# Kernel tuning notes

Hardware: AMD Instinct MI355X
Metric: run time of the kernel (lower is better)

Reference implementation:

```python
import jax, jax.numpy as jnp
import numpy as np
import math

B, N, DIM = 4, 2048, 512
HEADS, DIM_HEAD = 8, 64
INNER = HEADS * DIM_HEAD  # 512


def setup_inputs() -> dict:
    key = jax.random.key(0)
    ks = jax.random.split(key, 4)
    x = jax.random.normal(ks[0], (B, N, DIM), dtype=jnp.float32)
    # nn.Linear(dim, inner*4, bias=False): store as [dim, 4*inner] for x @ W
    w_qkvg = jax.random.normal(ks[1], (DIM, 4 * INNER), dtype=jnp.float32) * (1.0 / math.sqrt(DIM))
    sigma = jnp.full((1, HEADS, 1, 1), 1.92, dtype=jnp.float32)
    w_out = jax.random.normal(ks[2], (2 * INNER, DIM), dtype=jnp.float32) * (1.0 / math.sqrt(2 * INNER))
    b_out = jax.random.normal(ks[3], (DIM,), dtype=jnp.float32) * 0.01
    return {"x": x, "w_qkvg": w_qkvg, "sigma": sigma, "w_out": w_out, "b_out": b_out}


def reference(x, w_qkvg, sigma, w_out, b_out):
    b, n, d = x.shape
    h, dh = HEADS, DIM_HEAD
    scale = dh ** (-0.5)

    qkvg = x @ w_qkvg  # [b, n, 4*inner]
    q, k, vg, vsigma = jnp.split(qkvg, 4, axis=-1)

    def to_heads(t):  # [b, n, h*dh] -> [b, h, n, dh]
        return t.reshape(b, n, h, dh).transpose(0, 2, 1, 3)

    q, k, vg, vsigma = map(to_heads, (q, k, vg, vsigma))

    # --- softmax branch ---
    dots = jnp.einsum('bhid,bhjd->bhij', q, k) * scale  # [b, h, n, n]
    corr_g = jax.nn.softmax(dots, axis=-1)
    out_g = jnp.matmul(corr_g, vg)  # [b, h, n, dh]

    # --- Gaussian positional-mask branch ---
    pos = jnp.arange(1, n + 1, dtype=x.dtype)
    diffs = jnp.abs(pos[:, None] - pos[None, :])  # [n, n]
    inv_norm = 1.0 / (jnp.sqrt(jnp.asarray(2.0 * math.pi, x.dtype)) * sigma)  # [1, h, 1, 1]
    gm = inv_norm * jnp.exp(-(diffs ** 2)[None, None] / (2.0 * sigma ** 2))  # [1, h, n, n]
    corr_sigma = gm / gm.sum(-1, keepdims=True)
    out_s = jnp.matmul(corr_sigma, vsigma)  # broadcasts over batch -> [b, h, n, dh]

    out = jnp.concatenate([out_g, out_s], axis=-1)  # [b, h, n, 2*dh]
    out = out.transpose(0, 2, 1, 3).reshape(b, n, 2 * h * dh)
    return out @ w_out + b_out
```

## Files before the change

### kernel.cpp

```cpp
#include <hip/hip_runtime.h>

typedef _Float16 f16;
typedef __attribute__((ext_vector_type(8))) _Float16 f16x8;
typedef __attribute__((ext_vector_type(4))) _Float16 f16x4;
typedef __attribute__((ext_vector_type(4))) float f32x4;

#define B_ 4
#define N_ 2048
#define DIM_ 512
#define H_ 8
#define DH_ 64

__device__ __forceinline__ void gload16(const void* g, void* l) {
    __builtin_amdgcn_global_load_lds((const __attribute__((address_space(1))) void*)g,
                                     (__attribute__((address_space(3))) void*)l, 16, 0, 0);
}


__global__ __launch_bounds__(256) void cvt_f16_k8(const float* __restrict__ in,
                                                  f16* __restrict__ out, int n8) {
    int i = blockIdx.x * 256 + threadIdx.x;
    if (i < n8) {
        const float4 a = ((const float4*)in)[i * 2];
        const float4 b = ((const float4*)in)[i * 2 + 1];
        f16x8 o = {(f16)a.x, (f16)a.y, (f16)a.z, (f16)a.w,
                   (f16)b.x, (f16)b.y, (f16)b.z, (f16)b.w};
        ((f16x8*)out)[i] = o;
    }
}

__global__ __launch_bounds__(256) void transpose_cvt_k(const float* __restrict__ in,
                                                       f16* __restrict__ out, int K, int N) {
    __shared__ f16 tile[64][72];
    const int nbk = K >> 6;
    const int bk = blockIdx.x % nbk, bn = blockIdx.x / nbk;
    const int k0 = bk << 6, n0 = bn << 6;
    const int t = threadIdx.x;
    const int r = t >> 2, q = (t & 3) << 4;
#pragma unroll
    for (int u = 0; u < 4; u++) {
        const float4 v = *(const float4*)&in[(size_t)(k0 + r) * N + n0 + q + u * 4];
        tile[q + u * 4 + 0][r] = (f16)v.x;
        tile[q + u * 4 + 1][r] = (f16)v.y;
        tile[q + u * 4 + 2][r] = (f16)v.z;
        tile[q + u * 4 + 3][r] = (f16)v.w;
    }
    __syncthreads();
#pragma unroll
    for (int u = 0; u < 2; u++) {
        f16x8 o = *(const f16x8*)&tile[r][q + u * 8];
        *(f16x8*)&out[(size_t)(n0 + r) * K + k0 + q + u * 8] = o;
    }
}

__global__ __launch_bounds__(256) void gemm_bt0(
    const f16* __restrict__ A, const f16* __restrict__ BT, int K, int N,
    f16* __restrict__ qb, f16* __restrict__ kb, f16* __restrict__ vbT,
    f16* __restrict__ vs16)
{
    __shared__ char sAb[16384];
    __shared__ char sBb[16384];
    const int tid = threadIdx.x;
    const int bid = blockIdx.x;
    const int xcd = bid & 7, w = bid >> 3;
    const int m0 = ((xcd << 3) + (w >> 4)) << 7;
    const int n0 = (w & 15) << 7;
    const int wave = tid >> 6, lane = tid & 63;
    const int wr = wave >> 1, wc = wave & 1;
    const int lr = lane & 15, lg = lane >> 4;

    f32x4 acc[4][4];
    const f32x4 zero = {0.f, 0.f, 0.f, 0.f};
#pragma unroll
    for (int i = 0; i < 4; i++)
#pragma unroll
        for (int j = 0; j < 4; j++) acc[i][j] = zero;

    const f16* srcA[4]; const f16* srcB[4];
    char* ldsA[4]; char* ldsB[4];
#pragma unroll
    for (int u = 0; u < 4; u++) {
        int row = wave * 8 + u * 32 + (lane >> 3);
        int e0 = ((lane & 7) ^ (row & 7)) << 3;
        srcA[u] = A + (size_t)(m0 + row) * K + e0;
        srcB[u] = BT + (size_t)(n0 + row) * K + e0;
        ldsA[u] = sAb + wave * 1024 + u * 4096;
        ldsB[u] = sBb + wave * 1024 + u * 4096;
    }

    const int swz = (lr & 7) << 4;
    for (int kt = 0; kt < K; kt += 64) {
#pragma unroll
        for (int u = 0; u < 4; u++) {
            gload16(srcA[u], ldsA[u]);
            gload16(srcB[u], ldsB[u]);
            srcA[u] += 64; srcB[u] += 64;
        }
        __syncthreads();
#pragma unroll
        for (int half = 0; half < 2; half++) {
            f16x8 af[4], bf[4];
#pragma unroll
            for (int i = 0; i < 4; i++) {
                int R = wr * 64 + i * 16 + lr;
                af[i] = *(const f16x8*)(sAb + R * 128 + (((half << 6) | (lg << 4)) ^ swz));
            }
#pragma unroll
            for (int j = 0; j < 4; j++) {
                int R = wc * 64 + j * 16 + lr;
                bf[j] = *(const f16x8*)(sBb + R * 128 + (((half << 6) | (lg << 4)) ^ swz));
            }
#pragma unroll
            for (int i = 0; i < 4; i++)
#pragma unroll
                for (int j = 0; j < 4; j++)
                    acc[i][j] = __builtin_amdgcn_mfma_f32_16x16x32_f16(af[i], bf[j], acc[i][j], 0, 0, 0);
        }
        __syncthreads();
    }

#pragma unroll
    for (int i = 0; i < 4; i++) {
#pragma unroll
        for (int j = 0; j < 4; j++) {
            int col = n0 + wc * 64 + j * 16 + lr;
            int row0 = m0 + wr * 64 + i * 16 + lg * 4;
            int sec = col >> 9, cc = col & 511;
            int h = cc >> 6, d = cc & 63;
            int b = row0 >> 11, ns = row0 & 2047;
            if (sec == 2) {
                f16x4 o;
#pragma unroll
                for (int r = 0; r < 4; r++) o[r] = (f16)acc[i][j][r];
                *(f16x4*)&vbT[((size_t)(b * H_ + h) * DH_ + d) * N_ + ns] = o;
            } else if (sec == 0) {
#pragma unroll
                for (int r = 0; r < 4; r++)
                    qb[((size_t)(b * H_ + h) * N_ + ns + r) * DH_ + d] = (f16)(acc[i][j][r] * 0.1803368801f);
            } else if (sec == 1) {
#pragma unroll
                for (int r = 0; r < 4; r++)
                    kb[((size_t)(b * H_ + h) * N_ + ns + r) * DH_ + d] = (f16)acc[i][j][r];
            } else {
#pragma unroll
                for (int r = 0; r < 4; r++)
                    vs16[((size_t)(b * H_ + h) * N_ + ns + r) * DH_ + d] = (f16)acc[i][j][r];
            }
        }
    }
}

__global__ __launch_bounds__(256) void gemm_small(
    const f16* __restrict__ A, const f16* __restrict__ BT, int K, int N,
    const float* __restrict__ bias, float* __restrict__ outp)
{
    __shared__ char sAb[8192];
    __shared__ char sBb[8192];
    const int tid = threadIdx.x;
    const int bid = blockIdx.x;
    const int xcd = bid & 7, w = bid >> 3;
    const int m0 = ((xcd << 4) + (w >> 3)) << 6;
    const int n0 = (w & 7) << 6;
    const int wave = tid >> 6, lane = tid & 63;
    const int wr = wave >> 1, wc = wave & 1;
    const int lr = lane & 15, lg = lane >> 4;

    f32x4 acc[2][2];
    const f32x4 zero = {0.f, 0.f, 0.f, 0.f};
#pragma unroll
    for (int i = 0; i < 2; i++)
#pragma unroll
        for (int j = 0; j < 2; j++) acc[i][j] = zero;

    const f16* srcA[2]; const f16* srcB[2];
    char* ldsA[2]; char* ldsB[2];
#pragma unroll
    for (int u = 0; u < 2; u++) {
        int row = wave * 8 + u * 32 + (lane >> 3);
        int e0 = ((lane & 7) ^ (row & 7)) << 3;
        srcA[u] = A + (size_t)(m0 + row) * K + e0;
        srcB[u] = BT + (size_t)(n0 + row) * K + e0;
        ldsA[u] = sAb + wave * 1024 + u * 4096;
        ldsB[u] = sBb + wave * 1024 + u * 4096;
    }

    const int swz = (lr & 7) << 4;
    for (int kt = 0; kt < K; kt += 64) {
#pragma unroll
        for (int u = 0; u < 2; u++) {
            gload16(srcA[u], ldsA[u]);
            gload16(srcB[u], ldsB[u]);
            srcA[u] += 64; srcB[u] += 64;
        }
        __syncthreads();
#pragma unroll
        for (int half = 0; half < 2; half++) {
            f16x8 af[2], bf[2];
#pragma unroll
            for (int i = 0; i < 2; i++) {
                int R = wr * 32 + i * 16 + lr;
                af[i] = *(const f16x8*)(sAb + R * 128 + (((half << 6) | (lg << 4)) ^ swz));
            }
#pragma unroll
            for (int j = 0; j < 2; j++) {
                int R = wc * 32 + j * 16 + lr;
                bf[j] = *(const f16x8*)(sBb + R * 128 + (((half << 6) | (lg << 4)) ^ swz));
            }
#pragma unroll
            for (int i = 0; i < 2; i++)
#pragma unroll
                for (int j = 0; j < 2; j++)
                    acc[i][j] = __builtin_amdgcn_mfma_f32_16x16x32_f16(af[i], bf[j], acc[i][j], 0, 0, 0);
        }
        __syncthreads();
    }

#pragma unroll
    for (int i = 0; i < 2; i++)
#pragma unroll
        for (int j = 0; j < 2; j++) {
            int col = n0 + wc * 32 + j * 16 + lr;
            int row0 = m0 + wr * 32 + i * 16 + lg * 4;
#pragma unroll
            for (int r = 0; r < 4; r++)
                outp[(size_t)(row0 + r) * N + col] = acc[i][j][r] + bias[col];
        }
}

__global__ __launch_bounds__(256) void attn_k(
    const f16* __restrict__ qb, const f16* __restrict__ kb, const f16* __restrict__ vbT,
    f16* __restrict__ cat, f16* __restrict__ oaccB, float* __restrict__ lacc)
{
    __shared__ char sKbf[2 * 8192];
    __shared__ char sVbf[2 * 8192];
    const int tid = threadIdx.x;
    const int bid0 = blockIdx.x;
    const int obid = (bid0 & 7) * 128 + (bid0 >> 3);
    const int bh = obid >> 5, qblk = (obid >> 1) & 15, half = obid & 1;
    const int b = bh >> 3, h = bh & 7;
    const int hn = half << 4;
    const int wave = tid >> 6, lane = tid & 63;
    const int lr = lane & 15, lg = lane >> 4;

    const size_t base = (size_t)bh * N_ * DH_;
    const int qrow_a = qblk * 128 + wave * 32 + lr;
    const int qrow_b = qrow_a + 16;
    const f16x8 qfa0 = *(const f16x8*)&qb[base + (size_t)qrow_a * DH_ + lg * 8];
    const f16x8 qfa1 = *(const f16x8*)&qb[base + (size_t)qrow_a * DH_ + 32 + lg * 8];
    const f16x8 qfb0 = *(const f16x8*)&qb[base + (size_t)qrow_b * DH_ + lg * 8];
    const f16x8 qfb1 = *(const f16x8*)&qb[base + (size_t)qrow_b * DH_ + 32 + lg * 8];

    const f16* kq[2]; const f16* vq[2];
#pragma unroll
    for (int u = 0; u < 2; u++) {
        int row = wave * 8 + u * 32 + (lane >> 3);
        int e0 = ((lane & 7) ^ (row & 7)) << 3;
        kq[u] = kb + base + (size_t)row * 64 + e0;
        vq[u] = vbT + base + (size_t)row * 2048 + e0;
    }
    char* const ldsKw = sKbf + wave * 1024;
    char* const ldsVw = sVbf + wave * 1024;

    f32x4 Ota[4], Otb[4], lacc_a, lacc_b;
    const f32x4 zero = {0.f, 0.f, 0.f, 0.f};
#pragma unroll
    for (int dt = 0; dt < 4; dt++) { Ota[dt] = zero; Otb[dt] = zero; }
    lacc_a = zero; lacc_b = zero;
    const f16x8 ones8 = {(f16)1.f, (f16)1.f, (f16)1.f, (f16)1.f,
                         (f16)1.f, (f16)1.f, (f16)1.f, (f16)1.f};

    const int swz = (lr & 7) << 4;

#pragma unroll
    for (int u = 0; u < 2; u++) gload16(kq[u] + (size_t)hn * 4096, ldsKw + u * 4096);
#pragma unroll
    for (int u = 0; u < 2; u++) gload16(vq[u] + hn * 64, ldsVw + u * 4096);
    asm volatile("s_waitcnt vmcnt(0)" ::: "memory");
    __builtin_amdgcn_s_barrier();

    for (int t = 0; t < 16; t++) {
        {
            const int tn = hn + ((t + 1) & 15);
            char* vdst = ldsVw + ((t + 1) & 1) * 8192;
            char* kdst = ldsKw + ((t + 1) & 1) * 8192;
#pragma unroll
            for (int u = 0; u < 2; u++) gload16(vq[u] + tn * 64, vdst + u * 4096);
#pragma unroll
            for (int u = 0; u < 2; u++) gload16(kq[u] + (size_t)tn * 4096, kdst + u * 4096);
        }

        const char* Kb = sKbf + (t & 1) * 8192;
        const char* Vb = sVbf + (t & 1) * 8192;

        f32x4 sta[4], stb[4];
        __builtin_amdgcn_s_setprio(1);
#pragma unroll
        for (int ct = 0; ct < 4; ct++) {
            int row = ct * 16 + lr;
            f16x8 kf0 = *(const f16x8*)(Kb + (((row << 7) | (lg << 4)) ^ swz));
            f16x8 kf1 = *(const f16x8*)(Kb + (((row << 7) | 64 | (lg << 4)) ^ swz));
            f32x4 sa = __builtin_amdgcn_mfma_f32_16x16x32_f16(kf0, qfa0, zero, 0, 0, 0);
            sta[ct]  = __builtin_amdgcn_mfma_f32_16x16x32_f16(kf1, qfa1, sa, 0, 0, 0);
            f32x4 sb = __builtin_amdgcn_mfma_f32_16x16x32_f16(kf0, qfb0, zero, 0, 0, 0);
            stb[ct]  = __builtin_amdgcn_mfma_f32_16x16x32_f16(kf1, qfb1, sb, 0, 0, 0);
        }
        __builtin_amdgcn_s_setprio(0);

        f16x4 ppa[4], ppb[4];
#pragma unroll
        for (int ct = 0; ct < 4; ct++)
#pragma unroll
            for (int r = 0; r < 4; r++) {
                ppa[ct][r] = (f16)__builtin_amdgcn_exp2f(sta[ct][r]);
                ppb[ct][r] = (f16)__builtin_amdgcn_exp2f(stb[ct][r]);
            }

        __builtin_amdgcn_s_setprio(1);
#pragma unroll
        for (int c = 0; c < 2; c++) {
            f16x8 bfa = __builtin_shufflevector(ppa[2 * c], ppa[2 * c + 1], 0, 1, 2, 3, 4, 5, 6, 7);
            f16x8 bfb = __builtin_shufflevector(ppb[2 * c], ppb[2 * c + 1], 0, 1, 2, 3, 4, 5, 6, 7);
            lacc_a = __builtin_amdgcn_mfma_f32_16x16x32_f16(ones8, bfa, lacc_a, 0, 0, 0);
            lacc_b = __builtin_amdgcn_mfma_f32_16x16x32_f16(ones8, bfb, lacc_b, 0, 0, 0);
#pragma unroll
            for (int dt = 0; dt < 4; dt++) {
                int row = dt * 16 + lr;
                f16x4 vlo = *(const f16x4*)(Vb + (((row << 7) | (c << 6) | (lg << 3)) ^ swz));
                f16x4 vhi = *(const f16x4*)(Vb + (((row << 7) | (c << 6) | 32 | (lg << 3)) ^ swz));
                f16x8 vf = __builtin_shufflevector(vlo, vhi, 0, 1, 2, 3, 4, 5, 6, 7);
                Ota[dt] = __builtin_amdgcn_mfma_f32_16x16x32_f16(vf, bfa, Ota[dt], 0, 0, 0);
                Otb[dt] = __builtin_amdgcn_mfma_f32_16x16x32_f16(vf, bfb, Otb[dt], 0, 0, 0);
            }
        }
        __builtin_amdgcn_s_setprio(0);

        asm volatile("s_waitcnt vmcnt(0)" ::: "memory");
        __builtin_amdgcn_s_barrier();
    }

#pragma unroll
    for (int dt = 0; dt < 4; dt++) {
        f16x4 oa, ob;
#pragma unroll
        for (int r = 0; r < 4; r++) {
            oa[r] = (f16)Ota[dt][r];
            ob[r] = (f16)Otb[dt][r];
        }
        if (half == 0) {
            *(f16x4*)&cat[((size_t)(b * N_ + qrow_a)) * 1024 + h * 128 + dt * 16 + lg * 4] = oa;
            *(f16x4*)&cat[((size_t)(b * N_ + qrow_b)) * 1024 + h * 128 + dt * 16 + lg * 4] = ob;
        } else {
            *(f16x4*)&oaccB[((size_t)(bh * N_ + qrow_a)) * 64 + dt * 16 + lg * 4] = oa;
            *(f16x4*)&oaccB[((size_t)(bh * N_ + qrow_b)) * 64 + dt * 16 + lg * 4] = ob;
        }
    }
    if (lg == 0) {
        lacc[half * (32 * N_) + bh * N_ + qrow_a] = lacc_a[0];
        lacc[half * (32 * N_) + bh * N_ + qrow_b] = lacc_b[0];
    }
}

__global__ __launch_bounds__(256) void combine_k(
    f16* __restrict__ cat, const f16* __restrict__ oaccB, const float* __restrict__ lacc)
{
    int gi = blockIdx.x * 256 + threadIdx.x;
    int row = gi >> 3, c8 = gi & 7;
    int bh = row >> 11, q = row & 2047;
    int b = bh >> 3, h = bh & 7;
    float inv = 1.0f / (lacc[row] + lacc[32 * N_ + row]);
    f16* cp = &cat[((size_t)(b * N_ + q)) * 1024 + h * 128 + c8 * 8];
    f16x8 a = *(const f16x8*)cp;
    f16x8 o2 = *(const f16x8*)&oaccB[(size_t)row * 64 + c8 * 8];
    f16x8 o;
#pragma unroll
    for (int i = 0; i < 8; i++) o[i] = (f16)(((float)a[i] + (float)o2[i]) * inv);
    *(f16x8*)cp = o;
}

__global__ __launch_bounds__(256) void gauss_k(
    const f16* __restrict__ vs16, const float* __restrict__ sigma, f16* __restrict__ cat)
{
    const int tid = threadIdx.x;
    const int bh = blockIdx.y, b = bh >> 3, h = bh & 7;
    const int i0 = blockIdx.x * 64;
    const int wv = tid >> 6, d = tid & 63;
    const float sig = sigma[h];
    const float c = 0.72134752f / (sig * sig);

    float wt[17];
#pragma unroll
    for (int o = 0; o <= 16; o++) wt[o] = __builtin_amdgcn_exp2f(-(float)(o * o) * c);
    float wfull = wt[0];
#pragma unroll
    for (int o = 1; o <= 16; o++) wfull += 2.f * wt[o];
    const float inv_wfull = 1.0f / wfull;

    const size_t base = (size_t)bh * N_ * DH_;
    const int r0 = i0 + wv * 16 - 16;
    float v[48];
#pragma unroll
    for (int k = 0; k < 48; k++) {
        int r = r0 + k; r = r < 0 ? 0 : (r > N_ - 1 ? N_ - 1 : r);
        v[k] = (float)vs16[base + (size_t)r * DH_ + d];
    }

#pragma unroll
    for (int it = 0; it < 16; it++) {
        int i = i0 + wv * 16 + it;
        float acc = 0.f;
        if (i >= 16 && i <= N_ - 17) {
#pragma unroll
            for (int o = -16; o <= 16; o++)
                acc += wt[o < 0 ? -o : o] * v[16 + it + o];
            acc *= inv_wfull;
        } else {
            float ws = 0.f;
#pragma unroll
            for (int o = -16; o <= 16; o++) {
                int j = i + o;
                if (j >= 0 && j <= N_ - 1) {
                    float w = wt[o < 0 ? -o : o];
                    ws += w;
                    acc += w * v[16 + it + o];
                }
            }
            acc /= ws;
        }
        cat[((size_t)(b * N_ + i)) * 1024 + h * 128 + 64 + d] = (f16)acc;
    }
}


extern "C" void kernel_launch(void* const* d_in, const int* in_sizes, int n_in,
                              void* d_out, int out_size, void* d_ws, size_t ws_size,
                              hipStream_t stream) {
    const float* x      = (const float*)d_in[0];
    const float* w_qkvg = (const float*)d_in[1];
    const float* sigma  = (const float*)d_in[2];
    const float* w_out  = (const float*)d_in[3];
    const float* b_out  = (const float*)d_in[4];
    float* out = (float*)d_out;
    char* ws = (char*)d_ws;

    const size_t MB = 1048576;
    f16*   x16  = (f16*)(ws);
    float* lacc = (float*)(ws);
    f16*   wqT  = (f16*)(ws + 8 * MB);
    f16*   woT  = (f16*)(ws + 10 * MB);
    f16*   qb   = (f16*)(ws + 11 * MB);
    f16*   kb   = (f16*)(ws + 19 * MB);
    f16*   vbT  = (f16*)(ws + 27 * MB);
    f16*   vs16 = (f16*)(ws + 35 * MB);
    f16*   cat  = (f16*)(ws + 43 * MB);
    f16*   oaccB= (f16*)(ws + 59 * MB);
    if (ws_size < 67 * MB) return;

    cvt_f16_k8<<<2048, 256, 0, stream>>>(x, x16, B_ * N_ * DIM_ / 8);
    transpose_cvt_k<<<256, 256, 0, stream>>>(w_qkvg, wqT, 512, 2048);
    transpose_cvt_k<<<128, 256, 0, stream>>>(w_out, woT, 1024, 512);

    gemm_bt0<<<1024, 256, 0, stream>>>(x16, wqT, 512, 2048, qb, kb, vbT, vs16);

    attn_k<<<1024, 256, 0, stream>>>(qb, kb, vbT, cat, oaccB, lacc);
    combine_k<<<2048, 256, 0, stream>>>(cat, oaccB, lacc);
    gauss_k<<<dim3(32, 32), 256, 0, stream>>>(vs16, sigma, cat);

    gemm_small<<<1024, 256, 0, stream>>>(cat, woT, 1024, 512, b_out, out);
}
```

Measured before the change: 122.9 us.

## Rewrite QKV GEMM with 256x256 tiles and double-buffered phased LDS pipeline

Replaces the 128x128 QKV projection GEMM with a 512-thread kernel that computes 256x256 output tiles. Global-to-LDS loads for the next K step are double-buffered and spread across four barrier-separated phases, so memory traffic overlaps with MFMA work. Each phase raises wave priority around its MFMA block. The larger tiles give more operand reuse but use 128KB of LDS and 256 blocks, which limits occupancy to one block per CU. The final prefetch reads past the end of the valid K range into adjacent workspace memory, and that data is never used.

```diff
diff --git a/kernel.cpp b/kernel.cpp
--- a/kernel.cpp
+++ b/kernel.cpp
@@ -53,98 +53,123 @@
     }
 }
 
-__global__ __launch_bounds__(256) void gemm_bt0(
-    const f16* __restrict__ A, const f16* __restrict__ BT, int K, int N,
+__global__ __launch_bounds__(512, 2) void gemm0_8ph(
+    const f16* __restrict__ A, const f16* __restrict__ BT,
     f16* __restrict__ qb, f16* __restrict__ kb, f16* __restrict__ vbT,
     f16* __restrict__ vs16)
 {
-    __shared__ char sAb[16384];
-    __shared__ char sBb[16384];
+    __shared__ char lds[131072];
     const int tid = threadIdx.x;
     const int bid = blockIdx.x;
     const int xcd = bid & 7, w = bid >> 3;
-    const int m0 = ((xcd << 3) + (w >> 4)) << 7;
-    const int n0 = (w & 15) << 7;
+    const int m0 = ((xcd << 2) + (w >> 3)) << 8;
+    const int n0 = (w & 7) << 8;
     const int wave = tid >> 6, lane = tid & 63;
-    const int wr = wave >> 1, wc = wave & 1;
+    const int wr = wave >> 2, wc = wave & 3;
     const int lr = lane & 15, lg = lane >> 4;
 
-    f32x4 acc[4][4];
+    f32x4 acc[8][4];
     const f32x4 zero = {0.f, 0.f, 0.f, 0.f};
 #pragma unroll
-    for (int i = 0; i < 4; i++)
+    for (int i = 0; i < 8; i++)
 #pragma unroll
         for (int j = 0; j < 4; j++) acc[i][j] = zero;
 
-    const f16* srcA[4]; const f16* srcB[4];
-    char* ldsA[4]; char* ldsB[4];
-#pragma unroll
-    for (int u = 0; u < 4; u++) {
-        int row = wave * 8 + u * 32 + (lane >> 3);
-        int e0 = ((lane & 7) ^ (row & 7)) << 3;
-        srcA[u] = A + (size_t)(m0 + row) * K + e0;
-        srcB[u] = BT + (size_t)(n0 + row) * K + e0;
-        ldsA[u] = sAb + wave * 1024 + u * 4096;
-        ldsB[u] = sBb + wave * 1024 + u * 4096;
-    }
+    const f16* gA[2][2]; const f16* gB[2][2];
+#pragma unroll
+    for (int u = 0; u < 2; u++) {
+        int c = tid + u * 512;
+        int row = c >> 3;
+        int e0 = (((c & 7) ^ (row & 7)) << 3);
+#pragma unroll
+        for (int h = 0; h < 2; h++) {
+            gA[h][u] = A + (size_t)(m0 + h * 128 + row) * 512 + e0;
+            gB[h][u] = BT + (size_t)(n0 + h * 128 + row) * 512 + e0;
+        }
+    }
+    const int ldst = wave * 1024;
+
+#pragma unroll
+    for (int h = 0; h < 2; h++)
+#pragma unroll
+        for (int u = 0; u < 2; u++)
+            gload16(gA[h][u], lds + h * 16384 + ldst + u * 8192);
+#pragma unroll
+    for (int h = 0; h < 2; h++)
+#pragma unroll
+        for (int u = 0; u < 2; u++)
+            gload16(gB[h][u], lds + 65536 + h * 16384 + ldst + u * 8192);
 
     const int swz = (lr & 7) << 4;
-    for (int kt = 0; kt < K; kt += 64) {
-#pragma unroll
-        for (int u = 0; u < 4; u++) {
-            gload16(srcA[u], ldsA[u]);
-            gload16(srcB[u], ldsB[u]);
-            srcA[u] += 64; srcB[u] += 64;
-        }
-        __syncthreads();
-#pragma unroll
-        for (int half = 0; half < 2; half++) {
+    for (int T = 0; T < 8; T++) {
+        const int d = T & 1, d2 = (T + 1) & 1;
+        const size_t Tn64 = (size_t)(T + 1) * 64;
+        const char* Ab = lds + (d * 2 + wr) * 16384;
+        const char* Bb = lds + 65536 + (d * 2 + (wc >> 1)) * 16384;
+#pragma unroll
+        for (int p = 0; p < 4; p++) {
+            const int kh = p >> 1, qr = p & 1;
+            if (p < 2) {
+#pragma unroll
+                for (int u = 0; u < 2; u++)
+                    gload16(gA[p][u] + Tn64, lds + (d2 * 2 + p) * 16384 + ldst + u * 8192);
+            } else {
+#pragma unroll
+                for (int u = 0; u < 2; u++)
+                    gload16(gB[p - 2][u] + Tn64, lds + 65536 + (d2 * 2 + (p - 2)) * 16384 + ldst + u * 8192);
+            }
+            if (p == 0) {
+                asm volatile("s_waitcnt vmcnt(2)" ::: "memory");
+            }
+            __builtin_amdgcn_s_barrier();
+
             f16x8 af[4], bf[4];
-#pragma unroll
-            for (int i = 0; i < 4; i++) {
-                int R = wr * 64 + i * 16 + lr;
-                af[i] = *(const f16x8*)(sAb + R * 128 + (((half << 6) | (lg << 4)) ^ swz));
-            }
-#pragma unroll
-            for (int j = 0; j < 4; j++) {
-                int R = wc * 64 + j * 16 + lr;
-                bf[j] = *(const f16x8*)(sBb + R * 128 + (((half << 6) | (lg << 4)) ^ swz));
-            }
+            const int ko = (kh * 64 + lg * 16) ^ swz;
 #pragma unroll
             for (int i = 0; i < 4; i++)
+                af[i] = *(const f16x8*)(Ab + (qr * 64 + i * 16 + lr) * 128 + ko);
+#pragma unroll
+            for (int j = 0; j < 4; j++)
+                bf[j] = *(const f16x8*)(Bb + ((wc & 1) * 64 + j * 16 + lr) * 128 + ko);
+            asm volatile("s_waitcnt lgkmcnt(0)" ::: "memory");
+            __builtin_amdgcn_sched_barrier(0);
+            __builtin_amdgcn_s_setprio(1);
+#pragma unroll
+            for (int i = 0; i < 4; i++)
 #pragma unroll
                 for (int j = 0; j < 4; j++)
-                    acc[i][j] = __builtin_amdgcn_mfma_f32_16x16x32_f16(af[i], bf[j], acc[i][j], 0, 0, 0);
-        }
-        __syncthreads();
-    }
-
-#pragma unroll
-    for (int i = 0; i < 4; i++) {
+                    acc[qr * 4 + i][j] = __builtin_amdgcn_mfma_f32_16x16x32_f16(af[i], bf[j], acc[qr * 4 + i][j], 0, 0, 0);
+            __builtin_amdgcn_s_setprio(0);
+            __builtin_amdgcn_s_barrier();
+        }
+    }
+
+#pragma unroll
+    for (int fr = 0; fr < 8; fr++) {
 #pragma unroll
         for (int j = 0; j < 4; j++) {
             int col = n0 + wc * 64 + j * 16 + lr;
-            int row0 = m0 + wr * 64 + i * 16 + lg * 4;
+            int row0 = m0 + wr * 128 + fr * 16 + lg * 4;
             int sec = col >> 9, cc = col & 511;
-            int h = cc >> 6, d = cc & 63;
+            int h = cc >> 6, dd = cc & 63;
             int b = row0 >> 11, ns = row0 & 2047;
             if (sec == 2) {
                 f16x4 o;
 #pragma unroll
-                for (int r = 0; r < 4; r++) o[r] = (f16)acc[i][j][r];
-                *(f16x4*)&vbT[((size_t)(b * H_ + h) * DH_ + d) * N_ + ns] = o;
+                for (int r = 0; r < 4; r++) o[r] = (f16)acc[fr][j][r];
+                *(f16x4*)&vbT[((size_t)(b * H_ + h) * DH_ + dd) * N_ + ns] = o;
             } else if (sec == 0) {
 #pragma unroll
                 for (int r = 0; r < 4; r++)
-                    qb[((size_t)(b * H_ + h) * N_ + ns + r) * DH_ + d] = (f16)(acc[i][j][r] * 0.1803368801f);
+                    qb[((size_t)(b * H_ + h) * N_ + ns + r) * DH_ + dd] = (f16)(acc[fr][j][r] * 0.1803368801f);
             } else if (sec == 1) {
 #pragma unroll
                 for (int r = 0; r < 4; r++)
-                    kb[((size_t)(b * H_ + h) * N_ + ns + r) * DH_ + d] = (f16)acc[i][j][r];
+                    kb[((size_t)(b * H_ + h) * N_ + ns + r) * DH_ + dd] = (f16)acc[fr][j][r];
             } else {
 #pragma unroll
                 for (int r = 0; r < 4; r++)
-                    vs16[((size_t)(b * H_ + h) * N_ + ns + r) * DH_ + d] = (f16)acc[i][j][r];
+                    vs16[((size_t)(b * H_ + h) * N_ + ns + r) * DH_ + dd] = (f16)acc[fr][j][r];
             }
         }
     }
@@ -459,7 +484,7 @@
     transpose_cvt_k<<<256, 256, 0, stream>>>(w_qkvg, wqT, 512, 2048);
     transpose_cvt_k<<<128, 256, 0, stream>>>(w_out, woT, 1024, 512);
 
-    gemm_bt0<<<1024, 256, 0, stream>>>(x16, wqT, 512, 2048, qb, kb, vbT, vs16);
+    gemm0_8ph<<<256, 512, 0, stream>>>(x16, wqT, qb, kb, vbT, vs16);
 
     attn_k<<<1024, 256, 0, stream>>>(qb, kb, vbT, cat, oaccB, lacc);
     combine_k<<<2048, 256, 0, stream>>>(cat, oaccB, lacc);
```

New measurement: 120.8 us. Within noise of the previous version (-1.7%).
